# Optimization experiments

Measured on AMD Instinct MI355X. Metric: run time of the kernel, lower is better.

The kernel has to match this reference:

```python
import jax, jax.numpy as jnp
import numpy as np

N = 100000      # nodes
E = 1600000     # edges
F = 128         # num_node_features
C = 64          # graph_hidden_channels
NH = 256        # nhid
NOUT = 128      # nout
L = 4           # n_layers (hidden GCN layers)
G = 512         # number of graphs in batch


def setup_inputs() -> dict:
    key = jax.random.key(0)
    ks = jax.random.split(key, 10)
    x = jax.random.normal(ks[0], (N, F), jnp.float32)
    edge_index = jax.random.randint(ks[1], (2, E), 0, N, dtype=jnp.int64)
    batch = jnp.sort(jax.random.randint(ks[2], (N,), 0, G, dtype=jnp.int64))

    def w(k, shape, fan_in):
        return jax.random.normal(k, shape, jnp.float32) / np.float32(np.sqrt(fan_in))

    W0 = w(ks[3], (F, C), F)
    b0 = jnp.zeros((C,), jnp.float32)
    Wh = w(ks[4], (L, C, C), C)      # stacked hidden GCN weights
    bh = jnp.zeros((L, C), jnp.float32)
    W1 = w(ks[5], (C, NH), C)
    b1 = jnp.zeros((NH,), jnp.float32)
    W2 = w(ks[6], (NH, NOUT), NH)
    b2 = jnp.zeros((NOUT,), jnp.float32)
    return dict(x=x, edge_index=edge_index, batch=batch,
                W0=W0, b0=b0, Wh=Wh, bh=bh, W1=W1, b1=b1, W2=W2, b2=b2)


def _gcn_conv(h_in, W, b, src, dst, dinv):
    # PyG GCNConv: out_i = sum_{j->i} dinv_j * dinv_i * (x_j W) + dinv_i^2 * (x_i W) + b
    h = h_in @ W                                   # [N, C]
    coef = (dinv[src] * dinv[dst])[:, None]        # [E, 1]
    agg = jax.ops.segment_sum(h[src] * coef, dst, num_segments=N)
    agg = agg + h * (dinv * dinv)[:, None]         # self-loop term
    return agg + b


def reference(x, edge_index, batch, W0, b0, Wh, bh, W1, b1, W2, b2):
    src, dst = edge_index[0], edge_index[1]
    # degree with self loops (edge weight 1)
    deg = jax.ops.segment_sum(jnp.ones((E,), x.dtype), dst, num_segments=N) + 1.0
    dinv = jax.lax.rsqrt(deg)                      # [N]

    h = jax.nn.relu(_gcn_conv(x, W0, b0, src, dst, dinv))
    for i in range(L):
        h = jax.nn.relu(_gcn_conv(h, Wh[i], bh[i], src, dst, dinv))

    # global mean pool over graphs
    counts = jax.ops.segment_sum(jnp.ones((N,), x.dtype), batch, num_segments=G)
    pooled = jax.ops.segment_sum(h, batch, num_segments=G) / jnp.maximum(counts, 1.0)[:, None]

    out = jax.nn.relu(pooled @ W1 + b1)
    out = out @ W2 + b2
    return out
```

## Files before the change

### kernel.cpp

```cpp
#include <hip/hip_runtime.h>
#include <hip/hip_fp16.h>
#include <stddef.h>

static constexpr int Nn    = 100000;
static constexpr int Ee    = 1600000;
static constexpr int Ff    = 128;
static constexpr int Cc    = 64;
static constexpr int NHh   = 256;
static constexpr int NOUTt = 128;
static constexpr int Ll    = 4;
static constexpr int Gg    = 512;

static constexpr int SCAN_BLK = 1024;
static constexpr int NBLK_SCAN = (Nn + SCAN_BLK - 1) / SCAN_BLK;

static constexpr int NSUB   = (Nn + 511) / 512;
static constexpr int SUBCAP = 10240;

typedef _Float16 half8 __attribute__((ext_vector_type(8)));
typedef float    f32x4 __attribute__((ext_vector_type(4)));

__global__ __launch_bounds__(256) void bin_kernel(const int* __restrict__ src,
                                                  const int* __restrict__ dst,
                                                  int* __restrict__ sb,
                                                  int* __restrict__ scnt, int E) {
    __shared__ int lcnt[NSUB], lbase[NSUB];
    const int tid = threadIdx.x;
    for (int i = tid; i < NSUB; i += 256) lcnt[i] = 0;
    __syncthreads();
    const int base = blockIdx.x * 2048;
    int pk[8], ps[8], lr[8];
    #pragma unroll
    for (int i = 0; i < 8; ++i) {
        int e = base + i * 256 + tid;
        if (e < E) {
            int d = dst[e], s = src[e];
            int sub = d >> 9;
            ps[i] = sub;
            pk[i] = s | ((d & 511) << 17);
            lr[i] = atomicAdd(&lcnt[sub], 1);
        } else ps[i] = -1;
    }
    __syncthreads();
    for (int i = tid; i < NSUB; i += 256) lbase[i] = atomicAdd(&scnt[i], lcnt[i]);
    __syncthreads();
    #pragma unroll
    for (int i = 0; i < 8; ++i) {
        if (ps[i] >= 0) {
            int pos = lbase[ps[i]] + lr[i];
            if (pos < SUBCAP) sb[(size_t)ps[i] * SUBCAP + pos] = pk[i];
        }
    }
}

__global__ __launch_bounds__(512) void cnt3_kernel(const int* __restrict__ sb,
                                                   const int* __restrict__ scnt,
                                                   int* __restrict__ cnt,
                                                   float* __restrict__ dinv) {
    __shared__ int lcnt[512];
    const int sub = blockIdx.x, tid = threadIdx.x;
    lcnt[tid] = 0;
    __syncthreads();
    const int n = scnt[sub];
    const int* bp = sb + (size_t)sub * SUBCAP;
    for (int i = tid; i < n; i += 512) atomicAdd(&lcnt[(bp[i] >> 17) & 511], 1);
    __syncthreads();
    int node = sub * 512 + tid;
    if (node < Nn) {
        cnt[node] = lcnt[tid];
        dinv[node] = rsqrtf((float)lcnt[tid] + 1.0f);
    }
}

__global__ __launch_bounds__(SCAN_BLK) void scan1_kernel(const int* __restrict__ cnt,
                                                         int* __restrict__ row_off,
                                                         int* __restrict__ bsum, int n) {
    __shared__ int sd[SCAN_BLK];
    int tid = threadIdx.x;
    int gid = blockIdx.x * SCAN_BLK + tid;
    int v = (gid < n) ? cnt[gid] : 0;
    sd[tid] = v;
    __syncthreads();
    #pragma unroll
    for (int off = 1; off < SCAN_BLK; off <<= 1) {
        int t = (tid >= off) ? sd[tid - off] : 0;
        __syncthreads();
        sd[tid] += t;
        __syncthreads();
    }
    if (gid < n) row_off[gid + 1] = sd[tid];
    if (tid == SCAN_BLK - 1) bsum[blockIdx.x] = sd[tid];
}

__global__ __launch_bounds__(128) void scan2_kernel(const int* __restrict__ bsum,
                                                    int* __restrict__ boff, int nb) {
    __shared__ int sd[128];
    int tid = threadIdx.x;
    sd[tid] = (tid < nb) ? bsum[tid] : 0;
    __syncthreads();
    #pragma unroll
    for (int off = 1; off < 128; off <<= 1) {
        int t = (tid >= off) ? sd[tid - off] : 0;
        __syncthreads();
        sd[tid] += t;
        __syncthreads();
    }
    if (tid < nb) boff[tid] = (tid == 0) ? 0 : sd[tid - 1];
}

__global__ void scan3_kernel(int* __restrict__ row_off, const int* __restrict__ boff,
                             const int* __restrict__ batch, int* __restrict__ gstart, int n) {
    int gid = blockIdx.x * blockDim.x + threadIdx.x;
    if (gid < n) {
        row_off[gid + 1] += boff[gid >> 10];
        int bi = batch[gid];
        int bp = (gid == 0) ? -1 : batch[gid - 1];
        for (int g = bp + 1; g <= bi; ++g) gstart[g] = gid;
        if (gid == n - 1) {
            for (int g = bi + 1; g <= Gg; ++g) gstart[g] = n;
        }
    }
    if (gid == 0) row_off[0] = 0;
}

__global__ __launch_bounds__(512) void fill3_kernel(const int* __restrict__ sb,
                                                    const int* __restrict__ scnt,
                                                    const int* __restrict__ roff,
                                                    int* __restrict__ csr) {
    __shared__ int lcnt[512], lofs[512];
    __shared__ int gbase;
    const int sub = blockIdx.x, tid = threadIdx.x;
    lcnt[tid] = 0;
    if (tid == 0) gbase = roff[sub * 512];
    __syncthreads();
    const int n = scnt[sub];
    const int* bp = sb + (size_t)sub * SUBCAP;
    for (int i = tid; i < n; i += 512) atomicAdd(&lcnt[(bp[i] >> 17) & 511], 1);
    __syncthreads();
    int v = lcnt[tid];
    lofs[tid] = v;
    __syncthreads();
    #pragma unroll
    for (int off = 1; off < 512; off <<= 1) {
        int t = (tid >= off) ? lofs[tid - off] : 0;
        __syncthreads();
        lofs[tid] += t;
        __syncthreads();
    }
    int excl = lofs[tid] - v;
    __syncthreads();
    lcnt[tid] = excl;
    __syncthreads();
    for (int i = tid; i < n; i += 512) {
        int e = bp[i];
        int pos = atomicAdd(&lcnt[(e >> 17) & 511], 1);
        csr[gbase + pos] = e & 0x1FFFF;
    }
}

__global__ __launch_bounds__(512) void wcvt_kernel(const float* __restrict__ W0,
                                                   const float* __restrict__ Wh,
                                                   _Float16* __restrict__ Wf) {
    int t = blockIdx.x * blockDim.x + threadIdx.x;
    if (t < 1024) {
        int f = t >> 6, lane = t & 63;
        int ct = f >> 2, c = f & 3;
        _Float16* o = Wf + ((size_t)f * 64 + lane) * 8;
        int kbase = c * 32 + (lane >> 4) * 8;
        int col = ct * 16 + (lane & 15);
        #pragma unroll
        for (int j = 0; j < 8; ++j) o[j] = (_Float16)W0[(size_t)(kbase + j) * 64 + col];
    } else if (t < 1024 + 2048) {
        int u = t - 1024;
        int layer = u >> 9, rem = u & 511;
        int f = rem >> 6, lane = rem & 63;
        int ct = f >> 1, c = f & 1;
        _Float16* o = Wf + 8192 + (size_t)layer * 4096 + ((size_t)f * 64 + lane) * 8;
        int kbase = c * 32 + (lane >> 4) * 8;
        int col = ct * 16 + (lane & 15);
        #pragma unroll
        for (int j = 0; j < 8; ++j)
            o[j] = (_Float16)Wh[(size_t)layer * 4096 + (size_t)(kbase + j) * 64 + col];
    }
}

__global__ __launch_bounds__(256) void gemm0_mfma(const float* __restrict__ X,
                                                  const _Float16* __restrict__ Wf0,
                                                  const float* __restrict__ dinv,
                                                  __half* __restrict__ Y, int n) {
    __shared__ _Float16 lds[4][16 * 72];
    const int tid = threadIdx.x, lane = tid & 63, w = tid >> 6;
    const int wid = (blockIdx.x * 256 + tid) >> 6;
    if (wid >= (n >> 4)) return;
    const int node0 = wid * 16;

    half8 bf[16];
    #pragma unroll
    for (int f = 0; f < 16; ++f)
        bf[f] = *(const half8*)(Wf0 + ((size_t)f * 64 + lane) * 8);

    const float* xp = X + (size_t)(node0 + (lane & 15)) * Ff + (lane >> 4) * 8;
    f32x4 acc[4] = {};
    #pragma unroll
    for (int c = 0; c < 4; ++c) {
        float4 x0 = *(const float4*)(xp + c * 32);
        float4 x1 = *(const float4*)(xp + c * 32 + 4);
        half8 af;
        af[0] = (_Float16)x0.x; af[1] = (_Float16)x0.y; af[2] = (_Float16)x0.z; af[3] = (_Float16)x0.w;
        af[4] = (_Float16)x1.x; af[5] = (_Float16)x1.y; af[6] = (_Float16)x1.z; af[7] = (_Float16)x1.w;
        #pragma unroll
        for (int ct = 0; ct < 4; ++ct)
            acc[ct] = __builtin_amdgcn_mfma_f32_16x16x32_f16(af, bf[ct * 4 + c], acc[ct], 0, 0, 0);
    }

    const int r0 = (lane >> 4) * 4;
    float di[4];
    #pragma unroll
    for (int r = 0; r < 4; ++r) di[r] = dinv[node0 + r0 + r];
    #pragma unroll
    for (int ct = 0; ct < 4; ++ct)
        #pragma unroll
        for (int r = 0; r < 4; ++r)
            lds[w][(r0 + r) * 72 + ct * 16 + (lane & 15)] = (_Float16)(acc[ct][r] * di[r]);
    asm volatile("s_waitcnt lgkmcnt(0)" ::: "memory");
    #pragma unroll
    for (int p = 0; p < 2; ++p) {
        int row = p * 8 + (lane >> 3);
        int ch  = lane & 7;
        half8 v = *(const half8*)&lds[w][row * 72 + ch * 8];
        *(half8*)((_Float16*)Y + (size_t)(node0 + row) * 64 + ch * 8) = v;
    }
}

__global__ __launch_bounds__(256) void gemm_mfma(const __half* __restrict__ A16,
                                                 const _Float16* __restrict__ Wf,
                                                 const float* __restrict__ dinv,
                                                 __half* __restrict__ Y, int n) {
    __shared__ _Float16 lds[4][16 * 72];
    const int tid  = threadIdx.x;
    const int lane = tid & 63;
    const int w    = tid >> 6;
    const int wid  = (blockIdx.x * 256 + tid) >> 6;
    if (wid >= (n >> 4)) return;
    const int node0 = wid * 16;

    half8 bfrag[8];
    #pragma unroll
    for (int f = 0; f < 8; ++f)
        bfrag[f] = *(const half8*)(Wf + ((size_t)f * 64 + lane) * 8);

    const _Float16* Ap = (const _Float16*)A16 + (size_t)(node0 + (lane & 15)) * 64 + (lane >> 4) * 8;
    half8 afrag0 = *(const half8*)(Ap);
    half8 afrag1 = *(const half8*)(Ap + 32);

    f32x4 acc[4] = {};
    #pragma unroll
    for (int ct = 0; ct < 4; ++ct) {
        acc[ct] = __builtin_amdgcn_mfma_f32_16x16x32_f16(afrag0, bfrag[ct * 2 + 0], acc[ct], 0, 0, 0);
        acc[ct] = __builtin_amdgcn_mfma_f32_16x16x32_f16(afrag1, bfrag[ct * 2 + 1], acc[ct], 0, 0, 0);
    }

    const int r0 = (lane >> 4) * 4;
    float di[4];
    #pragma unroll
    for (int r = 0; r < 4; ++r) di[r] = dinv[node0 + r0 + r];

    #pragma unroll
    for (int ct = 0; ct < 4; ++ct)
        #pragma unroll
        for (int r = 0; r < 4; ++r)
            lds[w][(r0 + r) * 72 + ct * 16 + (lane & 15)] = (_Float16)(acc[ct][r] * di[r]);

    asm volatile("s_waitcnt lgkmcnt(0)" ::: "memory");

    #pragma unroll
    for (int p = 0; p < 2; ++p) {
        int row = p * 8 + (lane >> 3);
        int ch  = lane & 7;
        half8 v = *(const half8*)&lds[w][row * 72 + ch * 8];
        *(half8*)((_Float16*)Y + (size_t)(node0 + row) * 64 + ch * 8) = v;
    }
}

__device__ inline void add_h8(float acc[8], float4 raw) {
    const __half2* hp = reinterpret_cast<const __half2*>(&raw);
    #pragma unroll
    for (int j = 0; j < 4; ++j) {
        float2 f = __half22float2(hp[j]);
        acc[2 * j]     += f.x;
        acc[2 * j + 1] += f.y;
    }
}

__device__ inline void cvt_h8(float4 raw, float v[8]) {
    const __half2* hp = reinterpret_cast<const __half2*>(&raw);
    #pragma unroll
    for (int j = 0; j < 4; ++j) {
        float2 f = __half22float2(hp[j]);
        v[2 * j] = f.x; v[2 * j + 1] = f.y;
    }
}

__global__ __launch_bounds__(256) void gather_agg(const int* __restrict__ row_off,
                                                  const int* __restrict__ csr_src,
                                                  const float* __restrict__ dinv,
                                                  const __half* __restrict__ t,
                                                  const float* __restrict__ b,
                                                  __half* __restrict__ out, int n) {
    const int lane = threadIdx.x & 63;
    const int node = (blockIdx.x * blockDim.x + threadIdx.x) >> 6;
    if (node >= n) return;
    const int sub = lane >> 3;
    const int c8  = lane & 7;

    const int base = row_off[node];
    const int end  = row_off[node + 1];

    float acc[8] = {};

    for (int k0 = base; k0 < end; k0 += 64) {
        int myidx = (k0 + lane < end) ? csr_src[k0 + lane] : 0;
        int nk = min(64, end - k0);
        int k = 0;
        for (; k + 32 <= nk; k += 32) {
            int s0 = __shfl(myidx, k + sub);
            int s1 = __shfl(myidx, k + 8 + sub);
            int s2 = __shfl(myidx, k + 16 + sub);
            int s3 = __shfl(myidx, k + 24 + sub);
            float4 r0 = *(const float4*)(t + (size_t)s0 * 64 + c8 * 8);
            float4 r1 = *(const float4*)(t + (size_t)s1 * 64 + c8 * 8);
            float4 r2 = *(const float4*)(t + (size_t)s2 * 64 + c8 * 8);
            float4 r3 = *(const float4*)(t + (size_t)s3 * 64 + c8 * 8);
            add_h8(acc, r0);
            add_h8(acc, r1);
            add_h8(acc, r2);
            add_h8(acc, r3);
        }
        for (; k + 16 <= nk; k += 16) {
            int s0 = __shfl(myidx, k + sub);
            int s1 = __shfl(myidx, k + 8 + sub);
            float4 r0 = *(const float4*)(t + (size_t)s0 * 64 + c8 * 8);
            float4 r1 = *(const float4*)(t + (size_t)s1 * 64 + c8 * 8);
            add_h8(acc, r0);
            add_h8(acc, r1);
        }
        for (; k < nk; k += 8) {
            int kk = k + sub;
            int s = __shfl(myidx, kk);
            if (kk < nk) {
                float4 r = *(const float4*)(t + (size_t)s * 64 + c8 * 8);
                add_h8(acc, r);
            }
        }
    }

    #pragma unroll
    for (int off = 8; off < 64; off <<= 1) {
        #pragma unroll
        for (int j = 0; j < 8; ++j) acc[j] += __shfl_xor(acc[j], off);
    }

    if (sub == 0) {
        float di = dinv[node];
        float selfv[8];
        cvt_h8(*(const float4*)(t + (size_t)node * 64 + c8 * 8), selfv);
        float4 b0 = *(const float4*)(b + c8 * 8);
        float4 b1 = *(const float4*)(b + c8 * 8 + 4);
        float bb[8] = {b0.x, b0.y, b0.z, b0.w, b1.x, b1.y, b1.z, b1.w};
        __half2 o[4];
        #pragma unroll
        for (int j = 0; j < 4; ++j) {
            float v0 = fmaxf(di * (acc[2 * j]     + selfv[2 * j])     + bb[2 * j],     0.f);
            float v1 = fmaxf(di * (acc[2 * j + 1] + selfv[2 * j + 1]) + bb[2 * j + 1], 0.f);
            o[j] = __floats2half2_rn(v0, v1);
        }
        *(float4*)(out + (size_t)node * 64 + c8 * 8) = *reinterpret_cast<float4*>(o);
    }
}

__global__ __launch_bounds__(256) void pool_graph(const __half* __restrict__ h,
                                                  const int* __restrict__ gstart,
                                                  float* __restrict__ pooled) {
    __shared__ float sd[4][64];
    const int g    = blockIdx.x;
    const int lane = threadIdx.x & 63;
    const int wv   = threadIdx.x >> 6;
    const int s = gstart[g], e = gstart[g + 1];
    float acc = 0.f;
    for (int i = s + wv; i < e; i += 4) acc += __half2float(h[(size_t)i * 64 + lane]);
    sd[wv][lane] = acc;
    __syncthreads();
    if (wv == 0) {
        float sum = sd[0][lane] + sd[1][lane] + sd[2][lane] + sd[3][lane];
        float c = (float)(e - s);
        pooled[(size_t)g * 64 + lane] = sum / fmaxf(c, 1.f);
    }
}

__global__ void mlp1_kernel(const float* __restrict__ P, const float* __restrict__ W1,
                            const float* __restrict__ b1, float* __restrict__ H) {
    int gid = blockIdx.x * blockDim.x + threadIdx.x;
    if (gid >= Gg * NHh) return;
    int j = gid & (NHh - 1), g = gid >> 8;
    const float* p = P + (size_t)g * Cc;
    float s = b1[j];
    #pragma unroll 8
    for (int k = 0; k < Cc; ++k) s += p[k] * W1[(size_t)k * NHh + j];
    H[gid] = fmaxf(s, 0.f);
}

__global__ void mlp2_kernel(const float* __restrict__ H, const float* __restrict__ W2,
                            const float* __restrict__ b2, float* __restrict__ O) {
    int gid = blockIdx.x * blockDim.x + threadIdx.x;
    if (gid >= Gg * NOUTt) return;
    int j = gid & (NOUTt - 1), g = gid >> 7;
    const float* h = H + (size_t)g * NHh;
    float s = b2[j];
    #pragma unroll 8
    for (int k = 0; k < NHh; ++k) s += h[k] * W2[(size_t)k * NOUTt + j];
    O[gid] = s;
}

extern "C" void kernel_launch(void* const* d_in, const int* in_sizes, int n_in,
                              void* d_out, int out_size, void* d_ws, size_t ws_size,
                              hipStream_t stream) {
    const float* x     = (const float*)d_in[0];
    const int*   ei    = (const int*)  d_in[1];
    const int*   batch = (const int*)  d_in[2];
    const float* W0    = (const float*)d_in[3];
    const float* b0    = (const float*)d_in[4];
    const float* Wh    = (const float*)d_in[5];
    const float* bh    = (const float*)d_in[6];
    const float* W1    = (const float*)d_in[7];
    const float* b1    = (const float*)d_in[8];
    const float* W2    = (const float*)d_in[9];
    const float* b2    = (const float*)d_in[10];

    const int* src = ei;
    const int* dst = ei + Ee;

    char* ws = (char*)d_ws;
    constexpr size_t OFF_DINV  = 0;
    constexpr size_t OFF_CNT   = 400384;
    constexpr size_t OFF_ROFF  = OFF_CNT + 400384;
    constexpr size_t OFF_BSUM  = OFF_ROFF + 400384;
    constexpr size_t OFF_BOFF  = OFF_BSUM + 1024;
    constexpr size_t OFF_SCNT  = OFF_BOFF + 1024;
    constexpr size_t OFF_CSR   = OFF_SCNT + 1024;
    constexpr size_t OFF_T     = OFF_CSR + 6400256;
    constexpr size_t OFF_A     = OFF_T + 12800256;
    constexpr size_t OFF_POOL  = OFF_A + 12800256;
    constexpr size_t OFF_GST   = OFF_POOL + (size_t)Gg * Cc * 4;
    constexpr size_t OFF_HID   = OFF_GST + 4096;
    constexpr size_t OFF_WF    = OFF_HID + (size_t)Gg * NHh * 4;
    const size_t OFF_SB = OFF_T;

    float*    dinv   = (float*)   (ws + OFF_DINV);
    int*      cnt    = (int*)     (ws + OFF_CNT);
    int*      roff   = (int*)     (ws + OFF_ROFF);
    int*      bsum   = (int*)     (ws + OFF_BSUM);
    int*      boff   = (int*)     (ws + OFF_BOFF);
    int*      scnt   = (int*)     (ws + OFF_SCNT);
    int*      csrs   = (int*)     (ws + OFF_CSR);
    int*      sb     = (int*)     (ws + OFF_SB);
    __half*   T      = (__half*)  (ws + OFF_T);
    __half*   A      = (__half*)  (ws + OFF_A);
    float*    pooled = (float*)   (ws + OFF_POOL);
    int*      gstart = (int*)     (ws + OFF_GST);
    float*    hid    = (float*)   (ws + OFF_HID);
    _Float16* Wf     = (_Float16*)(ws + OFF_WF);
    _Float16* Wfh    = Wf + 8192;

    hipMemsetAsync(scnt, 0, 1024, stream);
    wcvt_kernel<<<6, 512, 0, stream>>>(W0, Wh, Wf);
    bin_kernel<<<(Ee + 2047) / 2048, 256, 0, stream>>>(src, dst, sb, scnt, Ee);
    cnt3_kernel<<<NSUB, 512, 0, stream>>>(sb, scnt, cnt, dinv);
    scan1_kernel<<<NBLK_SCAN, SCAN_BLK, 0, stream>>>(cnt, roff, bsum, Nn);
    scan2_kernel<<<1, 128, 0, stream>>>(bsum, boff, NBLK_SCAN);
    scan3_kernel<<<(Nn + 255) / 256, 256, 0, stream>>>(roff, boff, batch, gstart, Nn);
    fill3_kernel<<<NSUB, 512, 0, stream>>>(sb, scnt, roff, csrs);

    const int agg_blocks  = (Nn * 64 + 255) / 256;
    const int tile_blocks = ((Nn / 16) + 3) / 4;

    gemm0_mfma<<<tile_blocks, 256, 0, stream>>>(x, Wf, dinv, T, Nn);
    gather_agg<<<agg_blocks, 256, 0, stream>>>(roff, csrs, dinv, T, b0, A, Nn);

    for (int i = 0; i < Ll; ++i) {
        gemm_mfma<<<tile_blocks, 256, 0, stream>>>(A, Wfh + (size_t)i * 4096, dinv, T, Nn);
        gather_agg<<<agg_blocks, 256, 0, stream>>>(roff, csrs, dinv, T, bh + (size_t)i * Cc, A, Nn);
    }

    pool_graph<<<Gg, 256, 0, stream>>>(A, gstart, pooled);

    mlp1_kernel<<<(Gg * NHh + 255) / 256, 256, 0, stream>>>(pooled, W1, b1, hid);
    mlp2_kernel<<<(Gg * NOUTt + 255) / 256, 256, 0, stream>>>(hid, W2, b2, (float*)d_out);
}
```

Baseline: 359.3 us.

## Fuse degree count, scan, and CSR fill into one per-bucket kernel

Replaces the separate count, three-pass global scan, and fill kernels with a single kernel per 512-node bucket that writes CSR into padded per-bucket regions. Each node gets start and end offsets instead of a prefix-sum row pointer, so no global scan is needed, and dinv and graph start indices are computed in the same kernel. This removes four kernel launches and their serial dependencies, at the cost of a padded, non-contiguous CSR layout and an extra end-offset array read in the aggregation kernel.

```diff
diff --git a/kernel.cpp b/kernel.cpp
--- a/kernel.cpp
+++ b/kernel.cpp
@@ -10,9 +10,6 @@
 static constexpr int NOUTt = 128;
 static constexpr int Ll    = 4;
 static constexpr int Gg    = 512;
-
-static constexpr int SCAN_BLK = 1024;
-static constexpr int NBLK_SCAN = (Nn + SCAN_BLK - 1) / SCAN_BLK;
 
 static constexpr int NSUB   = (Nn + 511) / 512;
 static constexpr int SUBCAP = 10240;
@@ -53,85 +50,17 @@
     }
 }
 
-__global__ __launch_bounds__(512) void cnt3_kernel(const int* __restrict__ sb,
-                                                   const int* __restrict__ scnt,
-                                                   int* __restrict__ cnt,
-                                                   float* __restrict__ dinv) {
-    __shared__ int lcnt[512];
+__global__ __launch_bounds__(512) void fill_all(const int* __restrict__ sb,
+                                                const int* __restrict__ scnt,
+                                                const int* __restrict__ batch,
+                                                int* __restrict__ rs,
+                                                int* __restrict__ re,
+                                                float* __restrict__ dinv,
+                                                int* __restrict__ gstart,
+                                                int* __restrict__ csr) {
+    __shared__ int lcnt[512], lofs[512];
     const int sub = blockIdx.x, tid = threadIdx.x;
     lcnt[tid] = 0;
-    __syncthreads();
-    const int n = scnt[sub];
-    const int* bp = sb + (size_t)sub * SUBCAP;
-    for (int i = tid; i < n; i += 512) atomicAdd(&lcnt[(bp[i] >> 17) & 511], 1);
-    __syncthreads();
-    int node = sub * 512 + tid;
-    if (node < Nn) {
-        cnt[node] = lcnt[tid];
-        dinv[node] = rsqrtf((float)lcnt[tid] + 1.0f);
-    }
-}
-
-__global__ __launch_bounds__(SCAN_BLK) void scan1_kernel(const int* __restrict__ cnt,
-                                                         int* __restrict__ row_off,
-                                                         int* __restrict__ bsum, int n) {
-    __shared__ int sd[SCAN_BLK];
-    int tid = threadIdx.x;
-    int gid = blockIdx.x * SCAN_BLK + tid;
-    int v = (gid < n) ? cnt[gid] : 0;
-    sd[tid] = v;
-    __syncthreads();
-    #pragma unroll
-    for (int off = 1; off < SCAN_BLK; off <<= 1) {
-        int t = (tid >= off) ? sd[tid - off] : 0;
-        __syncthreads();
-        sd[tid] += t;
-        __syncthreads();
-    }
-    if (gid < n) row_off[gid + 1] = sd[tid];
-    if (tid == SCAN_BLK - 1) bsum[blockIdx.x] = sd[tid];
-}
-
-__global__ __launch_bounds__(128) void scan2_kernel(const int* __restrict__ bsum,
-                                                    int* __restrict__ boff, int nb) {
-    __shared__ int sd[128];
-    int tid = threadIdx.x;
-    sd[tid] = (tid < nb) ? bsum[tid] : 0;
-    __syncthreads();
-    #pragma unroll
-    for (int off = 1; off < 128; off <<= 1) {
-        int t = (tid >= off) ? sd[tid - off] : 0;
-        __syncthreads();
-        sd[tid] += t;
-        __syncthreads();
-    }
-    if (tid < nb) boff[tid] = (tid == 0) ? 0 : sd[tid - 1];
-}
-
-__global__ void scan3_kernel(int* __restrict__ row_off, const int* __restrict__ boff,
-                             const int* __restrict__ batch, int* __restrict__ gstart, int n) {
-    int gid = blockIdx.x * blockDim.x + threadIdx.x;
-    if (gid < n) {
-        row_off[gid + 1] += boff[gid >> 10];
-        int bi = batch[gid];
-        int bp = (gid == 0) ? -1 : batch[gid - 1];
-        for (int g = bp + 1; g <= bi; ++g) gstart[g] = gid;
-        if (gid == n - 1) {
-            for (int g = bi + 1; g <= Gg; ++g) gstart[g] = n;
-        }
-    }
-    if (gid == 0) row_off[0] = 0;
-}
-
-__global__ __launch_bounds__(512) void fill3_kernel(const int* __restrict__ sb,
-                                                    const int* __restrict__ scnt,
-                                                    const int* __restrict__ roff,
-                                                    int* __restrict__ csr) {
-    __shared__ int lcnt[512], lofs[512];
-    __shared__ int gbase;
-    const int sub = blockIdx.x, tid = threadIdx.x;
-    lcnt[tid] = 0;
-    if (tid == 0) gbase = roff[sub * 512];
     __syncthreads();
     const int n = scnt[sub];
     const int* bp = sb + (size_t)sub * SUBCAP;
@@ -147,7 +76,20 @@
         lofs[tid] += t;
         __syncthreads();
     }
-    int excl = lofs[tid] - v;
+    const int excl  = lofs[tid] - v;
+    const int gbase = sub * SUBCAP;
+    const int node  = sub * 512 + tid;
+    if (node < Nn) {
+        rs[node]   = gbase + excl;
+        re[node]   = gbase + excl + v;
+        dinv[node] = rsqrtf((float)v + 1.0f);
+        int bi = batch[node];
+        int bpv = (node == 0) ? -1 : batch[node - 1];
+        for (int g = bpv + 1; g <= bi; ++g) gstart[g] = node;
+        if (node == Nn - 1) {
+            for (int g = bi + 1; g <= Gg; ++g) gstart[g] = Nn;
+        }
+    }
     __syncthreads();
     lcnt[tid] = excl;
     __syncthreads();
@@ -301,20 +243,21 @@
     }
 }
 
-__global__ __launch_bounds__(256) void gather_agg(const int* __restrict__ row_off,
-                                                  const int* __restrict__ csr_src,
-                                                  const float* __restrict__ dinv,
-                                                  const __half* __restrict__ t,
-                                                  const float* __restrict__ b,
-                                                  __half* __restrict__ out, int n) {
+__global__ __launch_bounds__(256) void gather_agg2(const int* __restrict__ rs,
+                                                   const int* __restrict__ re,
+                                                   const int* __restrict__ csr_src,
+                                                   const float* __restrict__ dinv,
+                                                   const __half* __restrict__ t,
+                                                   const float* __restrict__ b,
+                                                   __half* __restrict__ out, int n) {
     const int lane = threadIdx.x & 63;
     const int node = (blockIdx.x * blockDim.x + threadIdx.x) >> 6;
     if (node >= n) return;
     const int sub = lane >> 3;
     const int c8  = lane & 7;
 
-    const int base = row_off[node];
-    const int end  = row_off[node + 1];
+    const int base = rs[node];
+    const int end  = re[node];
 
     float acc[8] = {};
 
@@ -440,26 +383,22 @@
     const int* dst = ei + Ee;
 
     char* ws = (char*)d_ws;
-    constexpr size_t OFF_DINV  = 0;
-    constexpr size_t OFF_CNT   = 400384;
-    constexpr size_t OFF_ROFF  = OFF_CNT + 400384;
-    constexpr size_t OFF_BSUM  = OFF_ROFF + 400384;
-    constexpr size_t OFF_BOFF  = OFF_BSUM + 1024;
-    constexpr size_t OFF_SCNT  = OFF_BOFF + 1024;
-    constexpr size_t OFF_CSR   = OFF_SCNT + 1024;
-    constexpr size_t OFF_T     = OFF_CSR + 6400256;
-    constexpr size_t OFF_A     = OFF_T + 12800256;
-    constexpr size_t OFF_POOL  = OFF_A + 12800256;
-    constexpr size_t OFF_GST   = OFF_POOL + (size_t)Gg * Cc * 4;
-    constexpr size_t OFF_HID   = OFF_GST + 4096;
-    constexpr size_t OFF_WF    = OFF_HID + (size_t)Gg * NHh * 4;
+    constexpr size_t OFF_DINV = 0;
+    constexpr size_t OFF_RS   = 400384;
+    constexpr size_t OFF_RE   = OFF_RS + 400384;
+    constexpr size_t OFF_SCNT = OFF_RE + 400384;
+    constexpr size_t OFF_CSR  = OFF_SCNT + 1024;
+    constexpr size_t OFF_T    = OFF_CSR + (size_t)NSUB * SUBCAP * 4;
+    constexpr size_t OFF_A    = OFF_T + 12800256;
+    constexpr size_t OFF_POOL = OFF_A + 12800256;
+    constexpr size_t OFF_GST  = OFF_POOL + (size_t)Gg * Cc * 4;
+    constexpr size_t OFF_HID  = OFF_GST + 4096;
+    constexpr size_t OFF_WF   = OFF_HID + (size_t)Gg * NHh * 4;
     const size_t OFF_SB = OFF_T;
 
     float*    dinv   = (float*)   (ws + OFF_DINV);
-    int*      cnt    = (int*)     (ws + OFF_CNT);
-    int*      roff   = (int*)     (ws + OFF_ROFF);
-    int*      bsum   = (int*)     (ws + OFF_BSUM);
-    int*      boff   = (int*)     (ws + OFF_BOFF);
+    int*      rs     = (int*)     (ws + OFF_RS);
+    int*      re     = (int*)     (ws + OFF_RE);
     int*      scnt   = (int*)     (ws + OFF_SCNT);
     int*      csrs   = (int*)     (ws + OFF_CSR);
     int*      sb     = (int*)     (ws + OFF_SB);
@@ -471,24 +410,20 @@
     _Float16* Wf     = (_Float16*)(ws + OFF_WF);
     _Float16* Wfh    = Wf + 8192;
 
-    hipMemsetAsync(scnt, 0, 1024, stream);
+    (void)hipMemsetAsync(scnt, 0, 1024, stream);
     wcvt_kernel<<<6, 512, 0, stream>>>(W0, Wh, Wf);
     bin_kernel<<<(Ee + 2047) / 2048, 256, 0, stream>>>(src, dst, sb, scnt, Ee);
-    cnt3_kernel<<<NSUB, 512, 0, stream>>>(sb, scnt, cnt, dinv);
-    scan1_kernel<<<NBLK_SCAN, SCAN_BLK, 0, stream>>>(cnt, roff, bsum, Nn);
-    scan2_kernel<<<1, 128, 0, stream>>>(bsum, boff, NBLK_SCAN);
-    scan3_kernel<<<(Nn + 255) / 256, 256, 0, stream>>>(roff, boff, batch, gstart, Nn);
-    fill3_kernel<<<NSUB, 512, 0, stream>>>(sb, scnt, roff, csrs);
+    fill_all<<<NSUB, 512, 0, stream>>>(sb, scnt, batch, rs, re, dinv, gstart, csrs);
 
     const int agg_blocks  = (Nn * 64 + 255) / 256;
     const int tile_blocks = ((Nn / 16) + 3) / 4;
 
     gemm0_mfma<<<tile_blocks, 256, 0, stream>>>(x, Wf, dinv, T, Nn);
-    gather_agg<<<agg_blocks, 256, 0, stream>>>(roff, csrs, dinv, T, b0, A, Nn);
+    gather_agg2<<<agg_blocks, 256, 0, stream>>>(rs, re, csrs, dinv, T, b0, A, Nn);
 
     for (int i = 0; i < Ll; ++i) {
         gemm_mfma<<<tile_blocks, 256, 0, stream>>>(A, Wfh + (size_t)i * 4096, dinv, T, Nn);
-        gather_agg<<<agg_blocks, 256, 0, stream>>>(roff, csrs, dinv, T, bh + (size_t)i * Cc, A, Nn);
+        gather_agg2<<<agg_blocks, 256, 0, stream>>>(rs, re, csrs, dinv, T, bh + (size_t)i * Cc, A, Nn);
     }
 
     pool_graph<<<Gg, 256, 0, stream>>>(A, gstart, pooled);
```

New measurement: 350.1 us. -2.6%, faster.
